# Performance work log

Hardware: AMD Instinct MI355X
Metric: run time of the kernel (lower is better)

## Reference

```python
import jax, jax.numpy as jnp
import numpy as np

N_NODES = 50000
N_EDGES = 800000
NUM_GRAPHS = 256
IN = 128
HID = 256
NUM_CLASSES = 10
EPS = 1e-5


def _glorot(key, shape):
    fan_in, fan_out = shape[0], shape[1]
    lim = (6.0 / (fan_in + fan_out)) ** 0.5
    return jax.random.uniform(key, shape, jnp.float32, -lim, lim)


def setup_inputs() -> dict:
    key = jax.random.key(0)
    ks = jax.random.split(key, 32)
    x = jax.random.normal(ks[0], (N_NODES, IN), jnp.float32)
    edge_index = jax.random.randint(ks[1], (2, N_EDGES), 0, N_NODES, jnp.int64)
    batch = jnp.sort(jax.random.randint(ks[2], (N_NODES,), 0, NUM_GRAPHS, jnp.int64))
    h = IN // 2  # 64
    p = {
        "x": x, "edge_index": edge_index, "batch": batch,
        # SAGEConv: out = lin_l(mean_aggr(x_j)) + lin_r(x_i); lin_l has bias, lin_r none
        "W1l": _glorot(ks[3], (IN, h)), "b1l": jnp.zeros((h,), jnp.float32), "W1r": _glorot(ks[4], (IN, h)),
        "W2l": _glorot(ks[5], (h, h)), "b2l": jnp.zeros((h,), jnp.float32), "W2r": _glorot(ks[6], (h, h)),
        "W3l": _glorot(ks[7], (h, h)), "b3l": jnp.zeros((h,), jnp.float32), "W3r": _glorot(ks[8], (h, h)),
        "lin1_w": _glorot(ks[9], (h, HID)), "lin1_b": jnp.zeros((HID,), jnp.float32),
        "g1": jnp.ones((HID,), jnp.float32), "be1": jnp.zeros((HID,), jnp.float32),
        "lin2_w": _glorot(ks[10], (HID, HID // 2)), "lin2_b": jnp.zeros((HID // 2,), jnp.float32),
        "g2": jnp.ones((HID // 2,), jnp.float32), "be2": jnp.zeros((HID // 2,), jnp.float32),
        "lin3_w": _glorot(ks[11], (HID // 2, HID // 4)), "lin3_b": jnp.zeros((HID // 4,), jnp.float32),
        "g3": jnp.ones((HID // 4,), jnp.float32), "be3": jnp.zeros((HID // 4,), jnp.float32),
        "lin4_w": _glorot(ks[12], (HID // 4, NUM_CLASSES)), "lin4_b": jnp.zeros((NUM_CLASSES,), jnp.float32),
    }
    return p


def sage_conv(x, src, dst, Wl, bl, Wr):
    # mean aggregation of source-node messages at destination nodes
    msg = x[src]  # [E, d] gather
    agg = jax.ops.segment_sum(msg, dst, num_segments=N_NODES)
    cnt = jax.ops.segment_sum(jnp.ones((src.shape[0],), x.dtype), dst, num_segments=N_NODES)
    agg = agg / jnp.maximum(cnt, 1.0)[:, None]
    return agg @ Wl + bl + x @ Wr


def batch_norm(x, gamma, beta):
    # training-mode BN (batch statistics, biased variance) as in torch default
    mean = jnp.mean(x, axis=0)
    var = jnp.mean((x - mean) ** 2, axis=0)
    return (x - mean) / jnp.sqrt(var + EPS) * gamma + beta


def reference(x, edge_index, batch,
              W1l, b1l, W1r, W2l, b2l, W2r, W3l, b3l, W3r,
              lin1_w, lin1_b, g1, be1, lin2_w, lin2_b, g2, be2,
              lin3_w, lin3_b, g3, be3, lin4_w, lin4_b):
    src, dst = edge_index[0], edge_index[1]
    h = sage_conv(x, src, dst, W1l, b1l, W1r)
    h = sage_conv(h, src, dst, W2l, b2l, W2r)
    h = sage_conv(h, src, dst, W3l, b3l, W3r)
    # global_mean_pool over graphs
    s = jax.ops.segment_sum(h, batch, num_segments=NUM_GRAPHS)
    n = jax.ops.segment_sum(jnp.ones((h.shape[0],), h.dtype), batch, num_segments=NUM_GRAPHS)
    c = s / jnp.maximum(n, 1.0)[:, None]
    # dropout is identity (self.training = False)
    c = jnp.tanh(batch_norm(c @ lin1_w + lin1_b, g1, be1))
    c = jnp.tanh(batch_norm(c @ lin2_w + lin2_b, g2, be2))
    c = jnp.tanh(batch_norm(c @ lin3_w + lin3_b, g3, be3))
    return c @ lin4_w + lin4_b
```

## Files before the change

### kernel.cpp

```cpp
#include <hip/hip_runtime.h>
#include <hip/hip_bf16.h>

#define N_NODES   50000
#define N_EDGES   800000
#define NUM_GRAPHS 256
#define IN_DIM    128
#define HD        64
#define EPS       1e-5f
#define SCAN_NB   196
#define NB_HEAD   64
#define GATHER_NB 12500

typedef __hip_bfloat16 bf16;

__global__ void k_diag(float* __restrict__ out, int n, float v) {
    int t = blockIdx.x * 256 + threadIdx.x;
    if (t < n) out[t] = v;
}

__global__ void k_count(const int* __restrict__ dst, const int* __restrict__ batch,
                        int* __restrict__ cnti, int* __restrict__ pos,
                        int* __restrict__ gb) {
    int e = blockIdx.x * 256 + threadIdx.x;
    if (e < N_EDGES) pos[e] = atomicAdd(&cnti[dst[e]], 1);
    if (e < N_NODES) {
        int bg = batch[e];
        int bnext = (e + 1 < N_NODES) ? batch[e + 1] : NUM_GRAPHS;
        if (e == 0) {
            for (int g = 0; g <= bg; ++g) gb[g] = 0;
        }
        for (int g = bg + 1; g <= bnext; ++g) gb[g] = e + 1;
    }
}

__global__ void k_scan1(const int* __restrict__ cnti, int* __restrict__ off,
                        int* __restrict__ bsum) {
    __shared__ int wsum[4];
    int idx = blockIdx.x * 256 + threadIdx.x;
    int lane = threadIdx.x & 63, wid = threadIdx.x >> 6;
    int v = (idx < N_NODES) ? cnti[idx] : 0;
    int s = v;
    #pragma unroll
    for (int o = 1; o < 64; o <<= 1) {
        int u = __shfl_up(s, o);
        if (lane >= o) s += u;
    }
    if (lane == 63) wsum[wid] = s;
    __syncthreads();
    int wbase = 0;
    #pragma unroll
    for (int w = 0; w < 4; w++) wbase += (w < wid) ? wsum[w] : 0;
    if (idx < N_NODES) off[idx] = wbase + s - v;
    if (threadIdx.x == 255) bsum[blockIdx.x] = wbase + s;
}

__global__ void k_scan3(int* __restrict__ off, const int* __restrict__ bsum,
                        const int* __restrict__ gb, float* __restrict__ invc) {
    __shared__ int wsum[4];
    __shared__ int spre;
    int lane = threadIdx.x & 63, wid = threadIdx.x >> 6;
    int v = (threadIdx.x < blockIdx.x) ? bsum[threadIdx.x] : 0;
    #pragma unroll
    for (int o = 32; o > 0; o >>= 1) v += __shfl_down(v, o);
    if (lane == 0) wsum[wid] = v;
    __syncthreads();
    if (threadIdx.x == 0) spre = wsum[0] + wsum[1] + wsum[2] + wsum[3];
    __syncthreads();
    int pre = spre;
    int idx = blockIdx.x * 256 + threadIdx.x;
    if (idx < N_NODES) off[idx] += pre;
    else if (idx == N_NODES) off[N_NODES] = N_EDGES;
    if (blockIdx.x == 0 && threadIdx.x < NUM_GRAPHS) {
        int c0 = gb[threadIdx.x], c1 = gb[threadIdx.x + 1];
        invc[threadIdx.x] = 1.0f / (float)max(c1 - c0, 1);
    }
}

__global__ void k_fill(const int* __restrict__ src, const int* __restrict__ dst,
                       const int* __restrict__ off, const int* __restrict__ pos,
                       int* __restrict__ nbr, int2* __restrict__ bounds) {
    int e = blockIdx.x * 256 + threadIdx.x;
    if (e < N_NODES) bounds[e] = make_int2(off[e], off[e + 1]);
    if (e >= N_EDGES) return;
    int d = dst[e];
    nbr[off[d] + pos[e]] = src[e];
}

template <int K, int NB>
__global__ __launch_bounds__(256) void k_xform3(
        const float* __restrict__ X, const float* __restrict__ Wl,
        const float* __restrict__ Wr, const float* __restrict__ bl,
        bf16* __restrict__ B, float* __restrict__ C) {
    __shared__ float tile[NB * K];
    const int NPW = NB / 4;
    int nodes0 = blockIdx.x * NB;
    {
        const int total4 = NB * K / 4;
        int nmax4 = (N_NODES - nodes0) * K / 4;
        const float4* Xg = (const float4*)(X + (long)nodes0 * K);
        float4* tg = (float4*)tile;
        for (int idx = threadIdx.x; idx < total4; idx += 256) {
            float4 v = make_float4(0.f, 0.f, 0.f, 0.f);
            if (idx < nmax4) v = Xg[idx];
            tg[idx] = v;
        }
    }
    __syncthreads();
    int wave = threadIdx.x >> 6, j = threadIdx.x & 63;
    long base = (long)nodes0 + wave * NPW;
    if (base >= N_NODES) return;
    float accB[NPW], accC[NPW];
    #pragma unroll
    for (int n = 0; n < NPW; n++) { accB[n] = 0.f; accC[n] = 0.f; }
    const float* Xs = tile + (wave * NPW) * K;
    for (int kc = 0; kc < K; kc += 4) {
        float wl0 = Wl[(kc + 0) * HD + j], wr0 = Wr[(kc + 0) * HD + j];
        float wl1 = Wl[(kc + 1) * HD + j], wr1 = Wr[(kc + 1) * HD + j];
        float wl2 = Wl[(kc + 2) * HD + j], wr2 = Wr[(kc + 2) * HD + j];
        float wl3 = Wl[(kc + 3) * HD + j], wr3 = Wr[(kc + 3) * HD + j];
        #pragma unroll
        for (int n = 0; n < NPW; n++) {
            float4 xv = *(const float4*)(Xs + n * K + kc);
            accB[n] = fmaf(xv.x, wl0, accB[n]);
            accC[n] = fmaf(xv.x, wr0, accC[n]);
            accB[n] = fmaf(xv.y, wl1, accB[n]);
            accC[n] = fmaf(xv.y, wr1, accC[n]);
            accB[n] = fmaf(xv.z, wl2, accB[n]);
            accC[n] = fmaf(xv.z, wr2, accC[n]);
            accB[n] = fmaf(xv.w, wl3, accB[n]);
            accC[n] = fmaf(xv.w, wr3, accC[n]);
        }
    }
    float bb = bl[j];
    int nact = (int)min((long)NPW, (long)N_NODES - base);
    for (int n = 0; n < nact; n++) {
        long i = base + n;
        B[i * HD + j] = __float2bfloat16(accB[n]);
        C[i * HD + j] = accC[n] + bb;
    }
}

__device__ __forceinline__ float bflo(unsigned u) { return __uint_as_float(u << 16); }
__device__ __forceinline__ float bfhi(unsigned u) { return __uint_as_float(u & 0xffff0000u); }

template <bool LAST>
__global__ __launch_bounds__(256) void k_gather(
        const int2* __restrict__ bounds, const int* __restrict__ nbr,
        const bf16* __restrict__ Bm, float* __restrict__ C,
        const int* __restrict__ batch, const float* __restrict__ invc,
        float* __restrict__ cb) {
    int h = blockIdx.x / GATHER_NB;
    int nb = blockIdx.x % GATHER_NB;
    int wid = threadIdx.x >> 6, lane = threadIdx.x & 63;
    int i = nb * 4 + wid;
    int q = lane >> 3, c = lane & 7;
    const uint2* B2 = (const uint2*)Bm;
    const long hb = (long)h * 8 + c;
    int2 be = bounds[i];
    int beg = be.x, end = be.y;
    float4 a0 = make_float4(0.f, 0.f, 0.f, 0.f);
    float4 a1 = make_float4(0.f, 0.f, 0.f, 0.f);
    float4 a2 = make_float4(0.f, 0.f, 0.f, 0.f);
    float4 a3 = make_float4(0.f, 0.f, 0.f, 0.f);
    for (int base = beg; base < end; base += 64) {
        int idx = base + lane;
        int nv = (idx < end) ? nbr[idx] : 0;
        int m = min(64, end - base);
        int tt = 0;
        for (; tt + 32 <= m; tt += 32) {
            int n0 = __shfl(nv, tt + q);
            int n1 = __shfl(nv, tt + 8 + q);
            int n2 = __shfl(nv, tt + 16 + q);
            int n3 = __shfl(nv, tt + 24 + q);
            uint2 u0 = B2[(long)n0 * 16 + hb];
            uint2 u1 = B2[(long)n1 * 16 + hb];
            uint2 u2 = B2[(long)n2 * 16 + hb];
            uint2 u3 = B2[(long)n3 * 16 + hb];
            a0.x += bflo(u0.x); a0.y += bfhi(u0.x); a0.z += bflo(u0.y); a0.w += bfhi(u0.y);
            a1.x += bflo(u1.x); a1.y += bfhi(u1.x); a1.z += bflo(u1.y); a1.w += bfhi(u1.y);
            a2.x += bflo(u2.x); a2.y += bfhi(u2.x); a2.z += bflo(u2.y); a2.w += bfhi(u2.y);
            a3.x += bflo(u3.x); a3.y += bfhi(u3.x); a3.z += bflo(u3.y); a3.w += bfhi(u3.y);
        }
        for (; tt + 16 <= m; tt += 16) {
            int n0 = __shfl(nv, tt + q);
            int n1 = __shfl(nv, tt + 8 + q);
            uint2 u0 = B2[(long)n0 * 16 + hb];
            uint2 u1 = B2[(long)n1 * 16 + hb];
            a0.x += bflo(u0.x); a0.y += bfhi(u0.x); a0.z += bflo(u0.y); a0.w += bfhi(u0.y);
            a1.x += bflo(u1.x); a1.y += bfhi(u1.x); a1.z += bflo(u1.y); a1.w += bfhi(u1.y);
        }
        for (; tt < m; tt += 8) {
            int n0 = __shfl(nv, tt + q);
            if (tt + q < m) {
                uint2 u0 = B2[(long)n0 * 16 + hb];
                a0.x += bflo(u0.x); a0.y += bfhi(u0.x);
                a0.z += bflo(u0.y); a0.w += bfhi(u0.y);
            }
        }
    }
    float4 s;
    s.x = (a0.x + a1.x) + (a2.x + a3.x);
    s.y = (a0.y + a1.y) + (a2.y + a3.y);
    s.z = (a0.z + a1.z) + (a2.z + a3.z);
    s.w = (a0.w + a1.w) + (a2.w + a3.w);
    s.x += __shfl_xor(s.x, 8); s.x += __shfl_xor(s.x, 16); s.x += __shfl_xor(s.x, 32);
    s.y += __shfl_xor(s.y, 8); s.y += __shfl_xor(s.y, 16); s.y += __shfl_xor(s.y, 32);
    s.z += __shfl_xor(s.z, 8); s.z += __shfl_xor(s.z, 16); s.z += __shfl_xor(s.z, 32);
    s.w += __shfl_xor(s.w, 8); s.w += __shfl_xor(s.w, 16); s.w += __shfl_xor(s.w, 32);
    int deg = end - beg;
    float inv = 1.0f / (float)max(deg, 1);
    if (!LAST) {
        if (lane < 8) {
            float4* Cp = (float4*)(C + (long)i * HD + h * 32 + 4 * lane);
            float4 cur = *Cp;
            cur.x += s.x * inv;
            cur.y += s.y * inv;
            cur.z += s.z * inv;
            cur.w += s.w * inv;
            *Cp = cur;
        }
    } else {
        __shared__ float red[4][32];
        __shared__ int gid[4];
        if (lane < 8) {
            const float4 cur = *(const float4*)(C + (long)i * HD + h * 32 + 4 * lane);
            red[wid][4 * lane + 0] = cur.x + s.x * inv;
            red[wid][4 * lane + 1] = cur.y + s.y * inv;
            red[wid][4 * lane + 2] = cur.z + s.z * inv;
            red[wid][4 * lane + 3] = cur.w + s.w * inv;
        }
        if (lane == 0) gid[wid] = batch[i];
        __syncthreads();
        if (wid == 0 && lane < 32) {
            int g0 = gid[0], g1 = gid[1], g2 = gid[2], g3 = gid[3];
            float v0 = red[0][lane], v1 = red[1][lane];
            float v2 = red[2][lane], v3 = red[3][lane];
            int col = h * 32 + lane;
            if (g0 == g3) {
                atomicAdd(&cb[g0 * HD + col],
                          ((v0 + v1) + (v2 + v3)) * invc[g0]);
            } else {
                atomicAdd(&cb[g0 * HD + col], v0 * invc[g0]);
                atomicAdd(&cb[g1 * HD + col], v1 * invc[g1]);
                atomicAdd(&cb[g2 * HD + col], v2 * invc[g2]);
                atomicAdd(&cb[g3 * HD + col], v3 * invc[g3]);
            }
        }
    }
}

__device__ __forceinline__ void gbar(int* bar, int round) {
    __syncthreads();
    if (threadIdx.x == 0) {
        __hip_atomic_fetch_add(bar, 1, __ATOMIC_ACQ_REL, __HIP_MEMORY_SCOPE_AGENT);
        int target = round * NB_HEAD;
        while (__hip_atomic_load(bar, __ATOMIC_ACQUIRE, __HIP_MEMORY_SCOPE_AGENT) < target) {}
    }
    __syncthreads();
}

__device__ __forceinline__ float ag_load(const float* p) {
    return __hip_atomic_load(p, __ATOMIC_RELAXED, __HIP_MEMORY_SCOPE_AGENT);
}

template <int NF>
__device__ __forceinline__ void stage4(float* __restrict__ s, const float* __restrict__ g) {
    const float4* g4 = (const float4*)g;
    float4* s4 = (float4*)s;
    #pragma unroll
    for (int i = 0; i < NF / 1024; i++)
        s4[i * 256 + threadIdx.x] = g4[i * 256 + threadIdx.x];
}

__global__ __launch_bounds__(256) void k_head(
        int* bar, float* __restrict__ gstat,
        const float* __restrict__ l1w, const float* __restrict__ l1b,
        const float* __restrict__ g1, const float* __restrict__ be1,
        const float* __restrict__ l2w, const float* __restrict__ l2b,
        const float* __restrict__ g2, const float* __restrict__ be2,
        const float* __restrict__ l3w, const float* __restrict__ l3b,
        const float* __restrict__ g3, const float* __restrict__ be3,
        const float* __restrict__ w4, const float* __restrict__ b4,
        const float* __restrict__ cb, float* __restrict__ out) {
    __shared__ float WB[32768];
    __shared__ float A1[4][64];
    __shared__ float A2[4][256];
    __shared__ float A3[4][128];
    __shared__ float M3[4][64];
    __shared__ float W4[640];
    float* gs1 = gstat;
    float* gq1 = gstat + 256;
    float* gs2 = gstat + 512;
    float* gq2 = gstat + 640;
    float* gs3 = gstat + 768;
    float* gq3 = gstat + 832;
    int t = threadIdx.x;
    int r0 = blockIdx.x * 4;

    {
        int r = t >> 6, lane = t & 63;
        A1[r][lane] = cb[(r0 + r) * HD + lane];
    }
    if (t < 160) ((float4*)W4)[t] = ((const float4*)w4)[t];
    stage4<16384>(WB + 16384, l1w);
    __syncthreads();

    float v1[4];
    {
        float bj = l1b[t];
        v1[0] = bj; v1[1] = bj; v1[2] = bj; v1[3] = bj;
        const float* Wp = WB + 16384;
        #pragma unroll 16
        for (int k = 0; k < 64; k++) {
            float w = Wp[k * 256 + t];
            v1[0] = fmaf(A1[0][k], w, v1[0]);
            v1[1] = fmaf(A1[1][k], w, v1[1]);
            v1[2] = fmaf(A1[2][k], w, v1[2]);
            v1[3] = fmaf(A1[3][k], w, v1[3]);
        }
        float s = (v1[0] + v1[1]) + (v1[2] + v1[3]);
        float q = (v1[0] * v1[0] + v1[1] * v1[1]) + (v1[2] * v1[2] + v1[3] * v1[3]);
        atomicAdd(&gs1[t], s);
        atomicAdd(&gq1[t], q);
    }
    __syncthreads();
    stage4<32768>(WB, l2w);
    gbar(bar, 1);
    {
        float S = ag_load(&gs1[t]), Q = ag_load(&gq1[t]);
        float mean = S * (1.0f / NUM_GRAPHS);
        float var = Q * (1.0f / NUM_GRAPHS) - mean * mean;
        float sc = rsqrtf(fmaxf(var, 0.f) + EPS) * g1[t];
        float sh = be1[t];
        #pragma unroll
        for (int r = 0; r < 4; r++)
            A2[r][t] = tanhf((v1[r] - mean) * sc + sh);
    }
    __syncthreads();

    float v2[2];
    int j2 = t & 127, rq2 = t >> 7;
    {
        float bj = l2b[j2];
        v2[0] = bj; v2[1] = bj;
        const float* a0 = A2[2 * rq2 + 0];
        const float* a1 = A2[2 * rq2 + 1];
        #pragma unroll 16
        for (int k = 0; k < 256; k++) {
            float w = WB[k * 128 + j2];
            v2[0] = fmaf(a0[k], w, v2[0]);
            v2[1] = fmaf(a1[k], w, v2[1]);
        }
        atomicAdd(&gs2[j2], v2[0] + v2[1]);
        atomicAdd(&gq2[j2], v2[0] * v2[0] + v2[1] * v2[1]);
    }
    __syncthreads();
    stage4<8192>(WB, l3w);
    gbar(bar, 2);
    {
        float S = ag_load(&gs2[j2]), Q = ag_load(&gq2[j2]);
        float mean = S * (1.0f / NUM_GRAPHS);
        float var = Q * (1.0f / NUM_GRAPHS) - mean * mean;
        float sc = rsqrtf(fmaxf(var, 0.f) + EPS) * g2[j2];
        float sh = be2[j2];
        A3[2 * rq2 + 0][j2] = tanhf((v2[0] - mean) * sc + sh);
        A3[2 * rq2 + 1][j2] = tanhf((v2[1] - mean) * sc + sh);
    }
    __syncthreads();

    float v3;
    int j3 = t & 63, rq3 = t >> 6;
    {
        float bj = l3b[j3];
        v3 = bj;
        const float* a = A3[rq3];
        #pragma unroll 16
        for (int k = 0; k < 128; k++) {
            float w = WB[k * 64 + j3];
            v3 = fmaf(a[k], w, v3);
        }
        atomicAdd(&gs3[j3], v3);
        atomicAdd(&gq3[j3], v3 * v3);
    }
    gbar(bar, 3);
    {
        float S = ag_load(&gs3[j3]), Q = ag_load(&gq3[j3]);
        float mean = S * (1.0f / NUM_GRAPHS);
        float var = Q * (1.0f / NUM_GRAPHS) - mean * mean;
        float sc = rsqrtf(fmaxf(var, 0.f) + EPS) * g3[j3];
        float sh = be3[j3];
        M3[rq3][j3] = tanhf((v3 - mean) * sc + sh);
    }
    __syncthreads();

    if (t < 40) {
        int q = t / 10, jf = t % 10;
        const float* rp = M3[q];
        float s = b4[jf];
        #pragma unroll
        for (int k = 0; k < 64; k++) s = fmaf(rp[k], W4[k * 10 + jf], s);
        out[(r0 + q) * 10 + jf] = s;
    }
}

extern "C" void kernel_launch(void* const* d_in, const int* in_sizes, int n_in,
                              void* d_out, int out_size, void* d_ws, size_t ws_size,
                              hipStream_t stream) {
    const float* x     = (const float*)d_in[0];
    const int*   ei    = (const int*) d_in[1];
    const int*   batch = (const int*) d_in[2];
    const float *W1l = (const float*)d_in[3],  *b1l = (const float*)d_in[4],  *W1r = (const float*)d_in[5];
    const float *W2l = (const float*)d_in[6],  *b2l = (const float*)d_in[7],  *W2r = (const float*)d_in[8];
    const float *W3l = (const float*)d_in[9],  *b3l = (const float*)d_in[10], *W3r = (const float*)d_in[11];
    const float *lin1_w = (const float*)d_in[12], *lin1_b = (const float*)d_in[13];
    const float *g1 = (const float*)d_in[14], *be1 = (const float*)d_in[15];
    const float *lin2_w = (const float*)d_in[16], *lin2_b = (const float*)d_in[17];
    const float *g2 = (const float*)d_in[18], *be2 = (const float*)d_in[19];
    const float *lin3_w = (const float*)d_in[20], *lin3_b = (const float*)d_in[21];
    const float *g3 = (const float*)d_in[22], *be3 = (const float*)d_in[23];
    const float *lin4_w = (const float*)d_in[24], *lin4_b = (const float*)d_in[25];

    const int* srcp = ei;
    const int* dstp = ei + N_EDGES;

    const long NF = (long)N_NODES * HD;
    char* wsb  = (char*)d_ws;
    int*  cnti = (int*)wsb;
    int*  bar  = cnti + 50048;
    float* gstat = (float*)(bar + 8);
    int*  pos  = (int*)(gstat + 896);
    int*  off  = pos  + 800000;
    int*  nbr  = off  + 50056;
    int*  bsum = nbr  + 800000;
    int*  gb   = bsum + 256;
    float* invc = (float*)(gb + 264);
    int2* bounds = (int2*)(invc + 256);
    bf16* B    = (bf16*)(bounds + 50000);
    float* H1  = (float*)(B + NF);
    float* H2  = H1  + NF;
    float* cb  = H2  + NF;
    float* endp= cb  + NUM_GRAPHS * HD;

    const size_t NEED = (size_t)((char*)endp - wsb);
    if (ws_size < NEED) {
        k_diag<<<(out_size + 255) / 256, 256, 0, stream>>>((float*)d_out, out_size,
                                                           (float)(ws_size >> 20));
        return;
    }

    const int TB = 256;
    const int gNE = (N_EDGES + TB - 1) / TB;
    const int gX16 = (N_NODES + 15) / 16;
    const int gGA = 2 * GATHER_NB;

    hipMemsetAsync(cnti, 0, (50048 + 8 + 896) * sizeof(int), stream);
    hipMemsetAsync(cb, 0, NUM_GRAPHS * HD * sizeof(float), stream);

    k_count<<<gNE, TB, 0, stream>>>(dstp, batch, cnti, pos, gb);
    k_scan1<<<SCAN_NB, TB, 0, stream>>>(cnti, off, bsum);
    k_scan3<<<SCAN_NB, TB, 0, stream>>>(off, bsum, gb, invc);
    k_fill<<<gNE, TB, 0, stream>>>(srcp, dstp, off, pos, nbr, bounds);

    k_xform3<IN_DIM, 16><<<gX16, TB, 0, stream>>>(x, W1l, W1r, b1l, B, H1);
    k_gather<false><<<gGA, TB, 0, stream>>>(bounds, nbr, B, H1, batch, invc, cb);
    k_xform3<HD, 16><<<gX16, TB, 0, stream>>>(H1, W2l, W2r, b2l, B, H2);
    k_gather<false><<<gGA, TB, 0, stream>>>(bounds, nbr, B, H2, batch, invc, cb);
    k_xform3<HD, 16><<<gX16, TB, 0, stream>>>(H2, W3l, W3r, b3l, B, H1);
    k_gather<true><<<gGA, TB, 0, stream>>>(bounds, nbr, B, H1, batch, invc, cb);

    k_head<<<NB_HEAD, TB, 0, stream>>>(bar, gstat,
                                       lin1_w, lin1_b, g1, be1,
                                       lin2_w, lin2_b, g2, be2,
                                       lin3_w, lin3_b, g3, be3,
                                       lin4_w, lin4_b,
                                       cb, (float*)d_out);
}
```

Measured before the change: 398.7 us.

## Split bf16 messages into half-feature planes, fuse count into first transform

Stores the bf16 message matrix as two separate 32-feature planes (low and high halves), so each gather block reads a compact 64-byte row per neighbor. Gather blocks are reordered so both halves of the same node group are scheduled close together, which should improve cache locality. Edge counting is folded into the first transform kernel (its grid of 3125×256 threads covers all 800k edges), bounds computation moves into the scan, and the cb memset moves into the scan, removing two launches and one memset. The fill kernel now uses the node-sized grid, which also exactly covers all edges.

```diff
diff --git a/kernel.cpp b/kernel.cpp
--- a/kernel.cpp
+++ b/kernel.cpp
@@ -9,28 +9,12 @@
 #define EPS       1e-5f
 #define SCAN_NB   196
 #define NB_HEAD   64
-#define GATHER_NB 12500
 
 typedef __hip_bfloat16 bf16;
 
 __global__ void k_diag(float* __restrict__ out, int n, float v) {
     int t = blockIdx.x * 256 + threadIdx.x;
     if (t < n) out[t] = v;
-}
-
-__global__ void k_count(const int* __restrict__ dst, const int* __restrict__ batch,
-                        int* __restrict__ cnti, int* __restrict__ pos,
-                        int* __restrict__ gb) {
-    int e = blockIdx.x * 256 + threadIdx.x;
-    if (e < N_EDGES) pos[e] = atomicAdd(&cnti[dst[e]], 1);
-    if (e < N_NODES) {
-        int bg = batch[e];
-        int bnext = (e + 1 < N_NODES) ? batch[e + 1] : NUM_GRAPHS;
-        if (e == 0) {
-            for (int g = 0; g <= bg; ++g) gb[g] = 0;
-        }
-        for (int g = bg + 1; g <= bnext; ++g) gb[g] = e + 1;
-    }
 }
 
 __global__ void k_scan1(const int* __restrict__ cnti, int* __restrict__ off,
@@ -55,7 +39,9 @@
 }
 
 __global__ void k_scan3(int* __restrict__ off, const int* __restrict__ bsum,
-                        const int* __restrict__ gb, float* __restrict__ invc) {
+                        const int* __restrict__ cnti, const int* __restrict__ gb,
+                        float* __restrict__ invc, int2* __restrict__ bounds,
+                        float* __restrict__ cb) {
     __shared__ int wsum[4];
     __shared__ int spre;
     int lane = threadIdx.x & 63, wid = threadIdx.x >> 6;
@@ -68,8 +54,14 @@
     __syncthreads();
     int pre = spre;
     int idx = blockIdx.x * 256 + threadIdx.x;
-    if (idx < N_NODES) off[idx] += pre;
-    else if (idx == N_NODES) off[N_NODES] = N_EDGES;
+    if (idx < N_NODES) {
+        int ofin = off[idx] + pre;
+        off[idx] = ofin;
+        bounds[idx] = make_int2(ofin, ofin + cnti[idx]);
+    } else if (idx == N_NODES) {
+        off[N_NODES] = N_EDGES;
+    }
+    if (blockIdx.x < 64) cb[blockIdx.x * 256 + threadIdx.x] = 0.f;
     if (blockIdx.x == 0 && threadIdx.x < NUM_GRAPHS) {
         int c0 = gb[threadIdx.x], c1 = gb[threadIdx.x + 1];
         invc[threadIdx.x] = 1.0f / (float)max(c1 - c0, 1);
@@ -78,19 +70,32 @@
 
 __global__ void k_fill(const int* __restrict__ src, const int* __restrict__ dst,
                        const int* __restrict__ off, const int* __restrict__ pos,
-                       int* __restrict__ nbr, int2* __restrict__ bounds) {
+                       int* __restrict__ nbr) {
     int e = blockIdx.x * 256 + threadIdx.x;
-    if (e < N_NODES) bounds[e] = make_int2(off[e], off[e + 1]);
     if (e >= N_EDGES) return;
     int d = dst[e];
     nbr[off[d] + pos[e]] = src[e];
 }
 
-template <int K, int NB>
+template <int K, int NB, bool CNT>
 __global__ __launch_bounds__(256) void k_xform3(
         const float* __restrict__ X, const float* __restrict__ Wl,
         const float* __restrict__ Wr, const float* __restrict__ bl,
-        bf16* __restrict__ B, float* __restrict__ C) {
+        bf16* __restrict__ Blo, bf16* __restrict__ Bhi, float* __restrict__ C,
+        const int* __restrict__ dst, const int* __restrict__ batch,
+        int* __restrict__ cnti, int* __restrict__ pos, int* __restrict__ gb) {
+    if (CNT) {
+        int e = blockIdx.x * 256 + threadIdx.x;
+        if (e < N_EDGES) pos[e] = atomicAdd(&cnti[dst[e]], 1);
+        if (e < N_NODES) {
+            int bg = batch[e];
+            int bnext = (e + 1 < N_NODES) ? batch[e + 1] : NUM_GRAPHS;
+            if (e == 0) {
+                for (int g = 0; g <= bg; ++g) gb[g] = 0;
+            }
+            for (int g = bg + 1; g <= bnext; ++g) gb[g] = e + 1;
+        }
+    }
     __shared__ float tile[NB * K];
     const int NPW = NB / 4;
     int nodes0 = blockIdx.x * NB;
@@ -132,10 +137,11 @@
         }
     }
     float bb = bl[j];
+    bf16* Bbase = (j < 32) ? (Blo + j) : (Bhi + (j - 32));
     int nact = (int)min((long)NPW, (long)N_NODES - base);
     for (int n = 0; n < nact; n++) {
         long i = base + n;
-        B[i * HD + j] = __float2bfloat16(accB[n]);
+        Bbase[i * 32] = __float2bfloat16(accB[n]);
         C[i * HD + j] = accC[n] + bb;
     }
 }
@@ -146,16 +152,17 @@
 template <bool LAST>
 __global__ __launch_bounds__(256) void k_gather(
         const int2* __restrict__ bounds, const int* __restrict__ nbr,
-        const bf16* __restrict__ Bm, float* __restrict__ C,
+        const bf16* __restrict__ Blo, const bf16* __restrict__ Bhi,
+        float* __restrict__ C,
         const int* __restrict__ batch, const float* __restrict__ invc,
         float* __restrict__ cb) {
-    int h = blockIdx.x / GATHER_NB;
-    int nb = blockIdx.x % GATHER_NB;
+    int grp = blockIdx.x >> 3, rr = blockIdx.x & 7;
+    int h = (rr >= 4) ? 1 : 0;
+    int nb = grp * 4 + (rr & 3);
     int wid = threadIdx.x >> 6, lane = threadIdx.x & 63;
     int i = nb * 4 + wid;
     int q = lane >> 3, c = lane & 7;
-    const uint2* B2 = (const uint2*)Bm;
-    const long hb = (long)h * 8 + c;
+    const uint2* B2 = (const uint2*)(h ? Bhi : Blo);
     int2 be = bounds[i];
     int beg = be.x, end = be.y;
     float4 a0 = make_float4(0.f, 0.f, 0.f, 0.f);
@@ -172,10 +179,10 @@
             int n1 = __shfl(nv, tt + 8 + q);
             int n2 = __shfl(nv, tt + 16 + q);
             int n3 = __shfl(nv, tt + 24 + q);
-            uint2 u0 = B2[(long)n0 * 16 + hb];
-            uint2 u1 = B2[(long)n1 * 16 + hb];
-            uint2 u2 = B2[(long)n2 * 16 + hb];
-            uint2 u3 = B2[(long)n3 * 16 + hb];
+            uint2 u0 = B2[(long)n0 * 8 + c];
+            uint2 u1 = B2[(long)n1 * 8 + c];
+            uint2 u2 = B2[(long)n2 * 8 + c];
+            uint2 u3 = B2[(long)n3 * 8 + c];
             a0.x += bflo(u0.x); a0.y += bfhi(u0.x); a0.z += bflo(u0.y); a0.w += bfhi(u0.y);
             a1.x += bflo(u1.x); a1.y += bfhi(u1.x); a1.z += bflo(u1.y); a1.w += bfhi(u1.y);
             a2.x += bflo(u2.x); a2.y += bfhi(u2.x); a2.z += bflo(u2.y); a2.w += bfhi(u2.y);
@@ -184,15 +191,15 @@
         for (; tt + 16 <= m; tt += 16) {
             int n0 = __shfl(nv, tt + q);
             int n1 = __shfl(nv, tt + 8 + q);
-            uint2 u0 = B2[(long)n0 * 16 + hb];
-            uint2 u1 = B2[(long)n1 * 16 + hb];
+            uint2 u0 = B2[(long)n0 * 8 + c];
+            uint2 u1 = B2[(long)n1 * 8 + c];
             a0.x += bflo(u0.x); a0.y += bfhi(u0.x); a0.z += bflo(u0.y); a0.w += bfhi(u0.y);
             a1.x += bflo(u1.x); a1.y += bfhi(u1.x); a1.z += bflo(u1.y); a1.w += bfhi(u1.y);
         }
         for (; tt < m; tt += 8) {
             int n0 = __shfl(nv, tt + q);
             if (tt + q < m) {
-                uint2 u0 = B2[(long)n0 * 16 + hb];
+                uint2 u0 = B2[(long)n0 * 8 + c];
                 a0.x += bflo(u0.x); a0.y += bfhi(u0.x);
                 a0.z += bflo(u0.y); a0.w += bfhi(u0.y);
             }
@@ -424,6 +431,7 @@
     const int* dstp = ei + N_EDGES;
 
     const long NF = (long)N_NODES * HD;
+    const long NH = (long)N_NODES * 32;
     char* wsb  = (char*)d_ws;
     int*  cnti = (int*)wsb;
     int*  bar  = cnti + 50048;
@@ -435,8 +443,9 @@
     int*  gb   = bsum + 256;
     float* invc = (float*)(gb + 264);
     int2* bounds = (int2*)(invc + 256);
-    bf16* B    = (bf16*)(bounds + 50000);
-    float* H1  = (float*)(B + NF);
+    bf16* Blo  = (bf16*)(bounds + 50000);
+    bf16* Bhi  = Blo + NH;
+    float* H1  = (float*)(Bhi + NH);
     float* H2  = H1  + NF;
     float* cb  = H2  + NF;
     float* endp= cb  + NUM_GRAPHS * HD;
@@ -449,24 +458,24 @@
     }
 
     const int TB = 256;
-    const int gNE = (N_EDGES + TB - 1) / TB;
     const int gX16 = (N_NODES + 15) / 16;
-    const int gGA = 2 * GATHER_NB;
+    const int gGA  = 25000;
 
     hipMemsetAsync(cnti, 0, (50048 + 8 + 896) * sizeof(int), stream);
-    hipMemsetAsync(cb, 0, NUM_GRAPHS * HD * sizeof(float), stream);
-
-    k_count<<<gNE, TB, 0, stream>>>(dstp, batch, cnti, pos, gb);
+
+    k_xform3<IN_DIM, 16, true><<<gX16, TB, 0, stream>>>(
+        x, W1l, W1r, b1l, Blo, Bhi, H1, dstp, batch, cnti, pos, gb);
     k_scan1<<<SCAN_NB, TB, 0, stream>>>(cnti, off, bsum);
-    k_scan3<<<SCAN_NB, TB, 0, stream>>>(off, bsum, gb, invc);
-    k_fill<<<gNE, TB, 0, stream>>>(srcp, dstp, off, pos, nbr, bounds);
-
-    k_xform3<IN_DIM, 16><<<gX16, TB, 0, stream>>>(x, W1l, W1r, b1l, B, H1);
-    k_gather<false><<<gGA, TB, 0, stream>>>(bounds, nbr, B, H1, batch, invc, cb);
-    k_xform3<HD, 16><<<gX16, TB, 0, stream>>>(H1, W2l, W2r, b2l, B, H2);
-    k_gather<false><<<gGA, TB, 0, stream>>>(bounds, nbr, B, H2, batch, invc, cb);
-    k_xform3<HD, 16><<<gX16, TB, 0, stream>>>(H2, W3l, W3r, b3l, B, H1);
-    k_gather<true><<<gGA, TB, 0, stream>>>(bounds, nbr, B, H1, batch, invc, cb);
+    k_scan3<<<SCAN_NB, TB, 0, stream>>>(off, bsum, cnti, gb, invc, bounds, cb);
+    k_fill<<<gX16, TB, 0, stream>>>(srcp, dstp, off, pos, nbr);
+
+    k_gather<false><<<gGA, TB, 0, stream>>>(bounds, nbr, Blo, Bhi, H1, batch, invc, cb);
+    k_xform3<HD, 16, false><<<gX16, TB, 0, stream>>>(
+        H1, W2l, W2r, b2l, Blo, Bhi, H2, nullptr, nullptr, nullptr, nullptr, nullptr);
+    k_gather<false><<<gGA, TB, 0, stream>>>(bounds, nbr, Blo, Bhi, H2, batch, invc, cb);
+    k_xform3<HD, 16, false><<<gX16, TB, 0, stream>>>(
+        H2, W3l, W3r, b3l, Blo, Bhi, H1, nullptr, nullptr, nullptr, nullptr, nullptr);
+    k_gather<true><<<gGA, TB, 0, stream>>>(bounds, nbr, Blo, Bhi, H1, batch, invc, cb);
 
     k_head<<<NB_HEAD, TB, 0, stream>>>(bar, gstat,
                                        lin1_w, lin1_b, g1, be1,
```

After: 375.7 us. 1.06x faster.
